# Kernel optimization log

Hardware: AMD Instinct MI355X
Metric: run time of the kernel (lower is better)

Reference implementation:

```python
import jax, jax.numpy as jnp
import numpy as np

N_ITER = 25
TOP_G = 0.07
BOT_G = 0.07
N_MIX = 1.0  # n=1 -> top target is exactly global_target


def _conv(x, W, b, stride):
    # NCHW valid conv, matching torch Conv2d
    y = jax.lax.conv_general_dilated(
        x, W, (stride, stride), 'VALID',
        dimension_numbers=('NCHW', 'OIHW', 'NCHW'))
    return y + b[None, :, None, None]


def setup_inputs() -> dict:
    key = jax.random.key(0)
    ks = jax.random.split(key, 8)
    B = 2048
    x = jax.random.normal(ks[0], (B, 3, 32, 32), jnp.float32)
    global_target = jax.random.uniform(ks[1], (B, 10), jnp.float32)

    def he(k, shape, fan_in):
        return jax.random.normal(k, shape, jnp.float32) * (1.0 / np.sqrt(fan_in))

    W1 = he(ks[2], (64, 3, 5, 5), 3 * 25);    b1 = jnp.zeros((64,), jnp.float32)
    W2 = he(ks[3], (128, 64, 5, 5), 64 * 25); b2 = jnp.zeros((128,), jnp.float32)
    W3 = he(ks[4], (256, 128, 3, 3), 128 * 9); b3 = jnp.zeros((256,), jnp.float32)
    W4 = he(ks[5], (10, 1024), 1024);          b4 = jnp.zeros((10,), jnp.float32)
    return {"x": x, "global_target": global_target,
            "W1": W1, "b1": b1, "W2": W2, "b2": b2,
            "W3": W3, "b3": b3, "W4": W4, "b4": b4}


def reference(x, global_target, W1, b1, W2, b2, W3, b3, W4, b4):
    B = x.shape[0]
    # layer functions (wts[0..3] in the torch module)
    f1 = lambda z: jax.nn.relu(_conv(z, W1, b1, 2))                      # [B,64,14,14]
    f2 = lambda z: jax.nn.relu(_conv(z, W2, b2, 2))                      # [B,128,5,5]
    f3 = lambda z: jax.nn.relu(_conv(z, W3, b3, 2)).reshape(z.shape[0], -1)  # [B,1024]
    f4 = lambda z: z @ W4.T + b4                                         # [B,10]

    # compute_values: feedforward pass
    h1 = f1(x); h2 = f2(h1); h3 = f3(h2); h4 = f4(h3)
    # top target: n*global_target + (1-n)*h4  (n=1)
    t4 = N_MIX * global_target + (1.0 - N_MIX) * h4

    # compute_PC_targets: iterative inference.
    # p[1] = wts[0](targ[0]) = f1(x) is constant == h1, so eps1 = t1 - h1.
    def step(carry, _):
        t1, t2, t3, p2, p3, p4 = carry
        e1 = t1 - h1
        e2 = t2 - p2
        e3 = t3 - p3
        e4 = (t4 - jax.nn.softmax(p4, axis=1)) * 0.5
        # epsdfdt = vjp of next layer at current target, cotangent = next eps
        _, v2 = jax.vjp(f2, t1); (g1,) = v2(e2)
        _, v3 = jax.vjp(f3, t2); (g2,) = v3(e3)
        _, v4 = jax.vjp(f4, t3); (g3,) = v4(e4)
        t1 = t1 + TOP_G * (-e1) + BOT_G * g1
        t2 = t2 + TOP_G * (-e2) + BOT_G * g2
        t3 = t3 + TOP_G * (-e3) + BOT_G * g3
        # recompute predictions from updated targets
        p2 = f2(t1); p3 = f3(t2); p4 = f4(t3)
        return (t1, t2, t3, p2, p3, p4), None

    carry0 = (h1, h2, h3, h2, h3, h4)
    (t1, t2, t3, _, _, _), _ = jax.lax.scan(step, carry0, None, length=N_ITER)

    # return refined PC targets (targ[1..3]; targ[0]=x and targ[4]=global_target are fixed)
    return jnp.concatenate(
        [t1.reshape(B, -1), t2.reshape(B, -1), t3.reshape(B, -1)], axis=1)
```

## Files before the change

kernel.cpp:

```cpp
#include <hip/hip_runtime.h>
#include <hip/hip_bf16.h>

typedef __hip_bfloat16 bf16;
typedef __attribute__((ext_vector_type(8))) short short8v;
typedef __attribute__((ext_vector_type(4))) float float4v;


__device__ __forceinline__ float b2f(bf16 v) { return __bfloat162float(v); }
__device__ __forceinline__ bf16  f2b(float v) { return __float2bfloat16(v); }
__device__ __forceinline__ float blo(unsigned u) { return __uint_as_float(u << 16); }
__device__ __forceinline__ float bhi(unsigned u) { return __uint_as_float(u & 0xffff0000u); }
__device__ __forceinline__ unsigned short fbits(float v) {
  union { bf16 b; unsigned short u; } c; c.b = f2b(v); return c.u;
}
__device__ __forceinline__ float ubf(unsigned short u) {
  return __uint_as_float(((unsigned)u) << 16);
}
__device__ __forceinline__ void gld16(const void* g, void* l) {
  __builtin_amdgcn_global_load_lds((const unsigned int*)g, (unsigned int*)l, 16, 0, 0);
}

__global__ __launch_bounds__(256) void k_prep(
    const float* __restrict__ W1, const float* __restrict__ W2,
    const float* __restrict__ W3, float* __restrict__ W1t,
    short* __restrict__ W2f, short* __restrict__ W2u,
    short* __restrict__ W3m, short* __restrict__ W3u) {
  int i = blockIdx.x * 256 + threadIdx.x;
  if (i < 4800) {
    int oc = i / 75, k = i % 75;
    W1t[k * 64 + oc] = W1[i];
  }
  if (i < 204800) {
    int oc = i / 1600, k = i % 1600, ic = k / 25, tap = k % 25;
    float w = W2[i];
    unsigned short hi = fbits(w);
    unsigned short lo = fbits(w - ubf(hi));
    W2f[(tap * 128 + oc) * 64 + (ic ^ ((oc & 7) << 3))] = (short)hi;
    W2f[204800 + (tap * 128 + oc) * 64 + (ic ^ ((oc & 7) << 3))] = (short)lo;
    W2u[(tap * 64 + ic) * 128 + (oc ^ ((ic & 7) << 3))] = (short)hi;
  }
  if (i < 294912) {
    int oc = i / 1152, k = i % 1152, ic = k / 9, tap = k % 9;
    float w = W3[i];
    unsigned short hi = fbits(w);
    unsigned short lo = fbits(w - ubf(hi));
    W3m[(tap * 256 + oc) * 128 + (ic ^ ((oc & 7) << 3))] = (short)hi;
    W3m[294912 + (tap * 256 + oc) * 128 + (ic ^ ((oc & 7) << 3))] = (short)lo;
    W3u[(tap * 128 + ic) * 256 + (oc ^ ((ic & 7) << 3))] = (short)hi;
  }
}

__global__ __launch_bounds__(512, 1) void k_conv1s(
    const float* __restrict__ x, const float* __restrict__ W1t,
    const float* __restrict__ b1, bf16* __restrict__ h1T) {
  __shared__ float xs[480 * 66];
  __shared__ float ws[4800];
  int bt = blockIdx.x, oy = blockIdx.y;
  int tid = threadIdx.x, lane = tid & 63, w8 = tid >> 6;
  int wv = w8 & 3, h = w8 >> 2;
  for (int i = tid; i < 4800; i += 512) ws[i] = W1t[i];
#pragma unroll
  for (int r = 0; r < 15; ++r) {
    int idx = r * 512 + tid;
    int col = idx / 120, q = idx % 120;
    int ic = q / 40, rem = q % 40;
    float4 v = *(const float4*)(x + (size_t)(bt * 64 + col) * 3072 +
                                ic * 1024 + oy * 64 + rem * 4);
    float* d = xs + (ic * 160 + rem * 4) * 66 + col;
    d[0] = v.x;
    d[66] = v.y;
    d[132] = v.z;
    d[198] = v.w;
  }
  __syncthreads();
  int oc0 = wv * 16;
  float acc[7][16];
#pragma unroll
  for (int o = 0; o < 7; ++o)
#pragma unroll
    for (int j = 0; j < 16; ++j) acc[o][j] = b1[oc0 + j];
  for (int ic = 0; ic < 3; ++ic)
    for (int ky = 0; ky < 5; ++ky) {
#pragma unroll
      for (int kx = 0; kx < 5; ++kx) {
        const float* wp = ws + ((ic * 25 + ky * 5 + kx) << 6) + oc0;
        float4 w0 = *(const float4*)(wp);
        float4 w1 = *(const float4*)(wp + 4);
        float4 w2 = *(const float4*)(wp + 8);
        float4 w3 = *(const float4*)(wp + 12);
        const float* xr = xs + (ic * 160 + ky * 32 + kx) * 66 + lane;
        float xv[7];
#pragma unroll
        for (int o = 0; o < 7; ++o) xv[o] = xr[(2 * (h * 7 + o)) * 66];
#pragma unroll
        for (int o = 0; o < 7; ++o) {
          float e = xv[o];
          acc[o][0] += e * w0.x;  acc[o][1] += e * w0.y;
          acc[o][2] += e * w0.z;  acc[o][3] += e * w0.w;
          acc[o][4] += e * w1.x;  acc[o][5] += e * w1.y;
          acc[o][6] += e * w1.z;  acc[o][7] += e * w1.w;
          acc[o][8] += e * w2.x;  acc[o][9] += e * w2.y;
          acc[o][10] += e * w2.z; acc[o][11] += e * w2.w;
          acc[o][12] += e * w3.x; acc[o][13] += e * w3.y;
          acc[o][14] += e * w3.z; acc[o][15] += e * w3.w;
        }
      }
    }
#pragma unroll
  for (int o = 0; o < 7; ++o) {
    int pix = oy * 14 + h * 7 + o;
    size_t tbase = ((size_t)(pix * 32 + bt)) << 12;
#pragma unroll
    for (int q = 0; q < 4; ++q) {
      ushort4 pk;
      pk.x = fbits(fmaxf(acc[o][q * 4 + 0], 0.f));
      pk.y = fbits(fmaxf(acc[o][q * 4 + 1], 0.f));
      pk.z = fbits(fmaxf(acc[o][q * 4 + 2], 0.f));
      pk.w = fbits(fmaxf(acc[o][q * 4 + 3], 0.f));
      int ocr = oc0 + q * 4;
      size_t off = tbase + lane * 64 + (ocr ^ ((lane & 7) << 3));
      *(ushort4*)(h1T + off) = pk;
    }
  }
}

__global__ __launch_bounds__(256) void k_fwd2m(
    const bf16* __restrict__ in1, const short* __restrict__ W2f,
    const float* __restrict__ b2, bf16* __restrict__ p2T,
    const bf16* __restrict__ t2e, bf16* __restrict__ e2T, int einit) {
  __shared__ __align__(16) short As0[8192];
  __shared__ __align__(16) short As1[8192];
  __shared__ __align__(16) short Bs[2][4096];
  int bid = blockIdx.x;
  int j = bid >> 3;
  int cbp = (bid & 7) * 2 + (j & 1), pos = j >> 1;
  int cb0 = cbp * 2;
  int tid = threadIdx.x, lane = tid & 63, wv = tid >> 6;
  int oy = pos / 5, ox = pos % 5;
  float4v acc[2][2][4];
#pragma unroll
  for (int c = 0; c < 2; ++c)
#pragma unroll
    for (int m = 0; m < 2; ++m)
#pragma unroll
      for (int n = 0; n < 4; ++n) acc[c][m][n] = (float4v){0.f, 0.f, 0.f, 0.f};

  for (int tap = 0; tap < 25; ++tap) {
    int ky = tap / 5, kx = tap % 5;
    int ipix = (2 * oy + ky) * 14 + (2 * ox + kx);
    __syncthreads();
    {
      const uint4* bs0 = (const uint4*)(in1 + (((size_t)(ipix * 32 + cb0)) << 12));
      const uint4* bs1 = (const uint4*)(in1 + (((size_t)(ipix * 32 + cb0 + 1)) << 12));
      uint4* bd = (uint4*)Bs;
      gld16(&bs0[tid], &bd[tid]);
      gld16(&bs0[tid + 256], &bd[tid + 256]);
      gld16(&bs1[tid], &bd[tid + 512]);
      gld16(&bs1[tid + 256], &bd[tid + 768]);
      const uint4* ah = (const uint4*)(W2f + tap * 8192);
      const uint4* al = (const uint4*)(W2f + 204800 + tap * 8192);
      uint4* dh = (uint4*)As0;
      uint4* dl = (uint4*)As1;
#pragma unroll
      for (int p = 0; p < 4; ++p) {
        gld16(&ah[tid + p * 256], &dh[tid + p * 256]);
        gld16(&al[tid + p * 256], &dl[tid + p * 256]);
      }
    }
    __syncthreads();
#pragma unroll
    for (int ks = 0; ks < 2; ++ks) {
      int ic0 = ks * 32 + ((lane >> 4) << 3);
      short8v bfr[2][4];
#pragma unroll
      for (int c = 0; c < 2; ++c)
#pragma unroll
        for (int n = 0; n < 4; ++n) {
          int colv = n * 16 + (lane & 15);
          bfr[c][n] = *(const short8v*)(&Bs[c][0] + colv * 64 + (ic0 ^ ((colv & 7) << 3)));
        }
#pragma unroll
      for (int m = 0; m < 2; ++m) {
        int row = wv * 32 + m * 16 + (lane & 15);
        int aoff = row * 64 + (ic0 ^ ((row & 7) << 3));
        short8v ah = *(const short8v*)(As0 + aoff);
        short8v al = *(const short8v*)(As1 + aoff);
#pragma unroll
        for (int c = 0; c < 2; ++c)
#pragma unroll
          for (int n = 0; n < 4; ++n) {
            acc[c][m][n] = __builtin_amdgcn_mfma_f32_16x16x32_bf16(ah, bfr[c][n], acc[c][m][n], 0, 0, 0);
            acc[c][m][n] = __builtin_amdgcn_mfma_f32_16x16x32_bf16(al, bfr[c][n], acc[c][m][n], 0, 0, 0);
          }
      }
    }
  }
#pragma unroll
  for (int c = 0; c < 2; ++c) {
    size_t tb2 = ((size_t)(pos * 32 + cb0 + c)) << 13;
#pragma unroll
    for (int m = 0; m < 2; ++m) {
      int ocb = wv * 32 + m * 16 + ((lane >> 4) << 2);
      float4 bv = *(const float4*)(b2 + ocb);
#pragma unroll
      for (int n = 0; n < 4; ++n) {
        int colv = n * 16 + (lane & 15);
        ushort4 pk;
        pk.x = fbits(fmaxf(acc[c][m][n][0] + bv.x, 0.f));
        pk.y = fbits(fmaxf(acc[c][m][n][1] + bv.y, 0.f));
        pk.z = fbits(fmaxf(acc[c][m][n][2] + bv.z, 0.f));
        pk.w = fbits(fmaxf(acc[c][m][n][3] + bv.w, 0.f));
        size_t off = tb2 + colv * 128 + (ocb ^ ((colv & 7) << 3));
        *(ushort4*)(p2T + off) = pk;
        if (einit) {
          ushort4 z = {0, 0, 0, 0};
          *(ushort4*)(e2T + off) = z;
        } else {
          ushort4 tv = *(const ushort4*)(t2e + off);
          ushort4 ev;
          float p0, t0;
          p0 = ubf(pk.x); t0 = ubf(tv.x); ev.x = fbits(p0 > 0.f ? t0 - p0 : 0.f);
          p0 = ubf(pk.y); t0 = ubf(tv.y); ev.y = fbits(p0 > 0.f ? t0 - p0 : 0.f);
          p0 = ubf(pk.z); t0 = ubf(tv.z); ev.z = fbits(p0 > 0.f ? t0 - p0 : 0.f);
          p0 = ubf(pk.w); t0 = ubf(tv.w); ev.w = fbits(p0 > 0.f ? t0 - p0 : 0.f);
          *(ushort4*)(e2T + off) = ev;
        }
      }
    }
  }
}

__global__ __launch_bounds__(256) void k_upd1m(
    const bf16* __restrict__ e2T, const short* __restrict__ W2u,
    const bf16* __restrict__ h1T, const bf16* __restrict__ t1r,
    bf16* __restrict__ t1w) {
  __shared__ __align__(16) short As0[8192];
  __shared__ __align__(16) short Es[2][8192];
  int bid = blockIdx.x;
  int j = bid >> 3;
  int cbp = (bid & 7) * 2 + (j & 1), pix = j >> 1;
  int cb0 = cbp * 2;
  int tid = threadIdx.x, lane = tid & 63, wv = tid >> 6;
  int iy = pix / 14, ix = pix % 14;
  float4v acc[2][4];
#pragma unroll
  for (int c = 0; c < 2; ++c)
#pragma unroll
    for (int n = 0; n < 4; ++n) acc[c][n] = (float4v){0.f, 0.f, 0.f, 0.f};

  for (int ky = iy & 1; ky <= 4; ky += 2) {
    int oy = (iy - ky) >> 1;
    if (oy < 0 || oy > 4) continue;
    for (int kx = ix & 1; kx <= 4; kx += 2) {
      int ox = (ix - kx) >> 1;
      if (ox < 0 || ox > 4) continue;
      int erow = oy * 5 + ox, tap = ky * 5 + kx;
      __syncthreads();
      {
        const uint4* es0 = (const uint4*)(e2T + (((size_t)(erow * 32 + cb0)) << 13));
        const uint4* es1 = (const uint4*)(e2T + (((size_t)(erow * 32 + cb0 + 1)) << 13));
        uint4* ed = (uint4*)Es;
        const uint4* ah = (const uint4*)(W2u + tap * 8192);
        uint4* dh = (uint4*)As0;
#pragma unroll
        for (int p = 0; p < 4; ++p) {
          gld16(&es0[tid + p * 256], &ed[tid + p * 256]);
          gld16(&es1[tid + p * 256], &ed[tid + p * 256 + 1024]);
          gld16(&ah[tid + p * 256], &dh[tid + p * 256]);
        }
      }
      __syncthreads();
#pragma unroll
      for (int ks = 0; ks < 4; ++ks) {
        int oc0 = ks * 32 + ((lane >> 4) << 3);
        int row = wv * 16 + (lane & 15);
        int aoff = row * 128 + (oc0 ^ ((row & 7) << 3));
        short8v ah = *(const short8v*)(As0 + aoff);
#pragma unroll
        for (int c = 0; c < 2; ++c)
#pragma unroll
          for (int n = 0; n < 4; ++n) {
            int colv = n * 16 + (lane & 15);
            short8v ef = *(const short8v*)(&Es[c][0] + colv * 128 + (oc0 ^ ((colv & 7) << 3)));
            acc[c][n] = __builtin_amdgcn_mfma_f32_16x16x32_bf16(ah, ef, acc[c][n], 0, 0, 0);
          }
      }
    }
  }
  int icb = wv * 16 + ((lane >> 4) << 2);
#pragma unroll
  for (int c = 0; c < 2; ++c) {
    size_t tb1 = ((size_t)(pix * 32 + cb0 + c)) << 12;
#pragma unroll
    for (int n = 0; n < 4; ++n) {
      int colv = n * 16 + (lane & 15);
      size_t off = tb1 + colv * 64 + (icb ^ ((colv & 7) << 3));
      ushort4 tv = *(const ushort4*)(t1r + off);
      ushort4 hv = *(const ushort4*)(h1T + off);
      ushort4 rp;
      float t0, h0;
      t0 = ubf(tv.x); h0 = ubf(hv.x);
      rp.x = fbits(t0 - 0.07f * (t0 - h0) + 0.07f * acc[c][n][0]);
      t0 = ubf(tv.y); h0 = ubf(hv.y);
      rp.y = fbits(t0 - 0.07f * (t0 - h0) + 0.07f * acc[c][n][1]);
      t0 = ubf(tv.z); h0 = ubf(hv.z);
      rp.z = fbits(t0 - 0.07f * (t0 - h0) + 0.07f * acc[c][n][2]);
      t0 = ubf(tv.w); h0 = ubf(hv.w);
      rp.w = fbits(t0 - 0.07f * (t0 - h0) + 0.07f * acc[c][n][3]);
      *(ushort4*)(t1w + off) = rp;
    }
  }
}

__global__ __launch_bounds__(256) void k_fwd3m(
    const bf16* __restrict__ in2, const short* __restrict__ W3m,
    const float* __restrict__ b3, bf16* __restrict__ p3T,
    const bf16* __restrict__ t3e, bf16* __restrict__ e3T, int einit) {
  __shared__ __align__(16) short As0[8192];
  __shared__ __align__(16) short As1[8192];
  __shared__ __align__(16) short Bs[8192];
  int bid = blockIdx.x;
  int j = bid >> 3;
  int cb = (bid & 7) * 4 + (j & 3);
  int r = j >> 2;
  int pos = r & 3, och = r >> 2;
  int tid = threadIdx.x, lane = tid & 63, wv = tid >> 6;
  int oy = pos >> 1, ox = pos & 1;
  float4v acc[4];
#pragma unroll
  for (int n = 0; n < 4; ++n) acc[n] = (float4v){0.f, 0.f, 0.f, 0.f};

  for (int tap = 0; tap < 9; ++tap) {
    int ky = tap / 3, kx = tap % 3;
    int irow = (2 * oy + ky) * 5 + (2 * ox + kx);
    __syncthreads();
    {
      const uint4* bs = (const uint4*)(in2 + (((size_t)(irow * 32 + cb)) << 13));
      uint4* bd = (uint4*)Bs;
#pragma unroll
      for (int p = 0; p < 4; ++p) gld16(&bs[tid + p * 256], &bd[tid + p * 256]);
      const uint4* ah = (const uint4*)(W3m + ((size_t)tap * 256 + och * 64) * 128);
      const uint4* al = (const uint4*)(W3m + 294912 + ((size_t)tap * 256 + och * 64) * 128);
      uint4* dh = (uint4*)As0;
      uint4* dl = (uint4*)As1;
#pragma unroll
      for (int p = 0; p < 4; ++p) {
        gld16(&ah[tid + p * 256], &dh[tid + p * 256]);
        gld16(&al[tid + p * 256], &dl[tid + p * 256]);
      }
    }
    __syncthreads();
#pragma unroll
    for (int ks = 0; ks < 4; ++ks) {
      int ic0 = ks * 32 + ((lane >> 4) << 3);
      short8v bfr[4];
#pragma unroll
      for (int n = 0; n < 4; ++n) {
        int colv = n * 16 + (lane & 15);
        bfr[n] = *(const short8v*)(Bs + colv * 128 + (ic0 ^ ((colv & 7) << 3)));
      }
      int row = wv * 16 + (lane & 15);
      int aoff = row * 128 + (ic0 ^ ((row & 7) << 3));
      short8v ah = *(const short8v*)(As0 + aoff);
      short8v al = *(const short8v*)(As1 + aoff);
#pragma unroll
      for (int n = 0; n < 4; ++n) {
        acc[n] = __builtin_amdgcn_mfma_f32_16x16x32_bf16(ah, bfr[n], acc[n], 0, 0, 0);
        acc[n] = __builtin_amdgcn_mfma_f32_16x16x32_bf16(al, bfr[n], acc[n], 0, 0, 0);
      }
    }
  }
  size_t tb3 = ((size_t)(pos * 32 + cb)) << 14;
  int ocg = och * 64 + wv * 16 + ((lane >> 4) << 2);
  float4 bv = *(const float4*)(b3 + ocg);
#pragma unroll
  for (int n = 0; n < 4; ++n) {
    int colv = n * 16 + (lane & 15);
    ushort4 pk;
    pk.x = fbits(fmaxf(acc[n][0] + bv.x, 0.f));
    pk.y = fbits(fmaxf(acc[n][1] + bv.y, 0.f));
    pk.z = fbits(fmaxf(acc[n][2] + bv.z, 0.f));
    pk.w = fbits(fmaxf(acc[n][3] + bv.w, 0.f));
    size_t off = tb3 + colv * 256 + (ocg ^ ((colv & 7) << 3));
    *(ushort4*)(p3T + off) = pk;
    if (einit) {
      ushort4 z = {0, 0, 0, 0};
      *(ushort4*)(e3T + off) = z;
    } else {
      ushort4 tv = *(const ushort4*)(t3e + off);
      ushort4 ev;
      float p0, t0;
      p0 = ubf(pk.x); t0 = ubf(tv.x); ev.x = fbits(p0 > 0.f ? t0 - p0 : 0.f);
      p0 = ubf(pk.y); t0 = ubf(tv.y); ev.y = fbits(p0 > 0.f ? t0 - p0 : 0.f);
      p0 = ubf(pk.z); t0 = ubf(tv.z); ev.z = fbits(p0 > 0.f ? t0 - p0 : 0.f);
      p0 = ubf(pk.w); t0 = ubf(tv.w); ev.w = fbits(p0 > 0.f ? t0 - p0 : 0.f);
      *(ushort4*)(e3T + off) = ev;
    }
  }
}

__global__ __launch_bounds__(256) void k_upd2m(
    const bf16* __restrict__ e3T, const bf16* __restrict__ p2T,
    const short* __restrict__ W3u, const bf16* __restrict__ t2r,
    bf16* __restrict__ t2w) {
  __shared__ __align__(16) short Es[8192];
  __shared__ __align__(16) short As0[16384];
  int bid = blockIdx.x;
  int j = bid >> 3;
  int cb = (bid & 7) * 4 + (j & 3), pix = j >> 2;
  int tid = threadIdx.x, lane = tid & 63, wv = tid >> 6;
  int iy = pix / 5, ix = pix % 5;
  float4v acc[2][4];
#pragma unroll
  for (int m = 0; m < 2; ++m)
#pragma unroll
    for (int n = 0; n < 4; ++n) acc[m][n] = (float4v){0.f, 0.f, 0.f, 0.f};

  for (int ky = iy & 1; ky <= 2; ky += 2) {
    int oy = (iy - ky) >> 1;
    if (oy < 0 || oy > 1) continue;
    for (int kx = ix & 1; kx <= 2; kx += 2) {
      int ox = (ix - kx) >> 1;
      if (ox < 0 || ox > 1) continue;
      int erow = oy * 2 + ox, tap = ky * 3 + kx;
      for (int occ = 0; occ < 2; ++occ) {
        __syncthreads();
        {
          size_t tb = ((size_t)(erow * 32 + cb)) << 14;
          uint4* ed = (uint4*)Es;
#pragma unroll
          for (int p = 0; p < 4; ++p) {
            int fi = tid + p * 256;
            int colr = fi >> 4, q = fi & 15;
            size_t g = tb + colr * 256 + occ * 128 + q * 8;
            gld16(e3T + g, &ed[fi]);
          }
          uint4* dh = (uint4*)As0;
#pragma unroll
          for (int p = 0; p < 8; ++p) {
            int fi = tid + p * 256;
            int icr = fi >> 4, q = fi & 15;
            size_t srcoff = ((size_t)(tap * 128 + icr)) * 256 + occ * 128 + q * 8;
            gld16(W3u + srcoff, &dh[fi]);
          }
        }
        __syncthreads();
#pragma unroll
        for (int ks = 0; ks < 4; ++ks) {
          int oc0 = ks * 32 + ((lane >> 4) << 3);
          short8v efr[4];
#pragma unroll
          for (int n = 0; n < 4; ++n) {
            int colv = n * 16 + (lane & 15);
            efr[n] = *(const short8v*)(Es + colv * 128 + (oc0 ^ ((colv & 7) << 3)));
          }
#pragma unroll
          for (int m = 0; m < 2; ++m) {
            int icr = wv * 32 + m * 16 + (lane & 15);
            int aoff = icr * 128 + (oc0 ^ ((icr & 7) << 3));
            short8v ah = *(const short8v*)(As0 + aoff);
#pragma unroll
            for (int n = 0; n < 4; ++n) {
              acc[m][n] = __builtin_amdgcn_mfma_f32_16x16x32_bf16(ah, efr[n], acc[m][n], 0, 0, 0);
            }
          }
        }
      }
    }
  }
  size_t tb2 = ((size_t)(pix * 32 + cb)) << 13;
#pragma unroll
  for (int m = 0; m < 2; ++m) {
    int icr = wv * 32 + m * 16 + ((lane >> 4) << 2);
#pragma unroll
    for (int n = 0; n < 4; ++n) {
      int colv = n * 16 + (lane & 15);
      size_t off = tb2 + colv * 128 + (icr ^ ((colv & 7) << 3));
      ushort4 tv = *(const ushort4*)(t2r + off);
      ushort4 pv = *(const ushort4*)(p2T + off);
      ushort4 rp;
      float t0, p0;
      t0 = ubf(tv.x); p0 = ubf(pv.x);
      rp.x = fbits(t0 - 0.07f * (t0 - p0) + 0.07f * acc[m][n][0]);
      t0 = ubf(tv.y); p0 = ubf(pv.y);
      rp.y = fbits(t0 - 0.07f * (t0 - p0) + 0.07f * acc[m][n][1]);
      t0 = ubf(tv.z); p0 = ubf(pv.z);
      rp.z = fbits(t0 - 0.07f * (t0 - p0) + 0.07f * acc[m][n][2]);
      t0 = ubf(tv.w); p0 = ubf(pv.w);
      rp.w = fbits(t0 - 0.07f * (t0 - p0) + 0.07f * acc[m][n][3]);
      *(ushort4*)(t2w + off) = rp;
    }
  }
}

__global__ __launch_bounds__(256) void k_fu3(
    const float* __restrict__ gt, const float* __restrict__ W4,
    const float* __restrict__ b4, const bf16* __restrict__ p3T,
    const bf16* __restrict__ t3r, bf16* __restrict__ t3w) {
  __shared__ __align__(16) float w4s[10560];
  int tid = threadIdx.x;
  for (int i = tid; i < 10240; i += 256) {
    int o = i >> 10, k = i & 1023;
    w4s[o * 1056 + k + ((k >> 7) << 2)] = W4[i];
  }
  __syncthreads();
  int c = blockIdx.x * 8 + (tid >> 5);
  int cb = c >> 6, colL = c & 63, subk = tid & 31;
  int pos = subk & 3, ch0 = (subk >> 2) * 32;
  int xc = (colL & 7) << 3;
  size_t boff = (((size_t)(pos * 32 + cb)) << 14) + colL * 256 + ch0;
  const bf16* trd = t3r + boff;
  const bf16* pb = p3T + boff;
  uint4 tq[4];
#pragma unroll
  for (int q = 0; q < 4; ++q) tq[q] = *(const uint4*)(trd + q * 8);
  float acc[10] = {};
#pragma unroll
  for (int q = 0; q < 4; ++q) {
    unsigned wds[4] = {tq[q].x, tq[q].y, tq[q].z, tq[q].w};
    int chb = (ch0 + q * 8) ^ xc;
#pragma unroll
    for (int h = 0; h < 4; ++h) {
      float v0 = blo(wds[h]), v1 = bhi(wds[h]);
      int k0 = (chb + 2 * h) * 4 + pos;
      int ks = k0 + ((k0 >> 7) << 2);
#pragma unroll
      for (int o = 0; o < 10; ++o)
        acc[o] += v0 * w4s[o * 1056 + ks] + v1 * w4s[o * 1056 + ks + 4];
    }
  }
#pragma unroll
  for (int off = 16; off > 0; off >>= 1)
#pragma unroll
    for (int o = 0; o < 10; ++o) acc[o] += __shfl_xor(acc[o], off, 32);
  float pv[10], m = -1e30f;
#pragma unroll
  for (int o = 0; o < 10; ++o) {
    pv[o] = acc[o] + b4[o];
    m = fmaxf(m, pv[o]);
  }
  float s = 0.f;
#pragma unroll
  for (int o = 0; o < 10; ++o) {
    pv[o] = __expf(pv[o] - m);
    s += pv[o];
  }
  float inv = 1.f / s;
  float e4[10];
#pragma unroll
  for (int o = 0; o < 10; ++o)
    e4[o] = (gt[(size_t)c * 10 + o] - pv[o] * inv) * 0.5f;
  bf16* tb = t3w + boff;
#pragma unroll
  for (int q = 0; q < 4; ++q) {
    uint4 pq = *(const uint4*)(pb + q * 8);
    unsigned tw[4] = {tq[q].x, tq[q].y, tq[q].z, tq[q].w};
    unsigned pw[4] = {pq.x, pq.y, pq.z, pq.w};
    int chb = (ch0 + q * 8) ^ xc;
    unsigned ro[4];
#pragma unroll
    for (int h = 0; h < 4; ++h) {
      int k0 = (chb + 2 * h) * 4 + pos;
      int ks = k0 + ((k0 >> 7) << 2);
      float g0 = 0.f, g1 = 0.f;
#pragma unroll
      for (int o = 0; o < 10; ++o) {
        g0 += e4[o] * w4s[o * 1056 + ks];
        g1 += e4[o] * w4s[o * 1056 + ks + 4];
      }
      float t0 = blo(tw[h]), p0 = blo(pw[h]);
      float t1 = bhi(tw[h]), p1 = bhi(pw[h]);
      float r0 = t0 - 0.07f * (t0 - p0) + 0.07f * g0;
      float r1 = t1 - 0.07f * (t1 - p1) + 0.07f * g1;
      ro[h] = (unsigned)fbits(r0) | ((unsigned)fbits(r1) << 16);
    }
    uint4 rv = {ro[0], ro[1], ro[2], ro[3]};
    *(uint4*)(tb + q * 8) = rv;
  }
}

__global__ __launch_bounds__(256) void k_tr1(
    const bf16* __restrict__ t1T, float* __restrict__ out) {
  __shared__ short lds[2 * 64 * 224];
  int cb = blockIdx.x, c0 = blockIdx.y * 2;
  int tid = threadIdx.x;
  for (int i = tid; i < 3136; i += 256) {
    int pix = i >> 4, q = i & 15;
    int colL = q >> 3, chb = (q & 7) << 3;
    int col = c0 + colL;
    uint4 v = *(const uint4*)(t1T + (((size_t)(pix * 32 + cb)) << 12) + col * 64 + chb);
    int icb = chb ^ ((col & 7) << 3);
    int posX = pix ^ (((icb >> 3) & 7) << 2);
    short* d = lds + (colL * 64 + icb) * 224 + posX;
    const short* vs = (const short*)&v;
#pragma unroll
    for (int j = 0; j < 8; ++j) d[j * 224] = vs[j];
  }
  __syncthreads();
  for (int i = tid; i < 6272; i += 256) {
    int colL = i / 3136, m = i % 3136;
    int ic = m / 49, pp = m % 49;
    int posX = (pp * 4) ^ (((ic >> 3) & 7) << 2);
    const short* s = lds + (colL * 64 + ic) * 224 + posX;
    float4 o;
    o.x = ubf((unsigned short)s[0]);
    o.y = ubf((unsigned short)s[1]);
    o.z = ubf((unsigned short)s[2]);
    o.w = ubf((unsigned short)s[3]);
    *(float4*)(out + ((size_t)(cb * 64 + c0 + colL)) * 16768 + m * 4) = o;
  }
}

__global__ __launch_bounds__(256) void k_tr2(
    const bf16* __restrict__ t2T, float* __restrict__ out) {
  __shared__ short lds[4 * 128 * 32];
  int cb = blockIdx.x, c0 = blockIdx.y * 4;
  int tid = threadIdx.x;
  for (int i = tid; i < 1600; i += 256) {
    int pos = i >> 6, q = i & 63;
    int colL = q >> 4, chb = (q & 15) << 3;
    int col = c0 + colL;
    uint4 v = *(const uint4*)(t2T + (((size_t)(pos * 32 + cb)) << 13) + col * 128 + chb);
    int ocb = chb ^ ((col & 7) << 3);
    int posX = pos ^ (((ocb >> 3) & 7) << 2);
    short* d = lds + (colL * 128 + ocb) * 32 + posX;
    const short* vs = (const short*)&v;
#pragma unroll
    for (int j = 0; j < 8; ++j) d[j * 32] = vs[j];
  }
  __syncthreads();
  for (int i = tid; i < 3200; i += 256) {
    int colL = i / 800, m = i % 800;
    int f0 = m * 4;
    float4 o;
    float* po = &o.x;
#pragma unroll
    for (int t = 0; t < 4; ++t) {
      int f = f0 + t;
      int oc = f / 25, pos = f % 25;
      int posX = pos ^ (((oc >> 3) & 7) << 2);
      po[t] = ubf((unsigned short)lds[(colL * 128 + oc) * 32 + posX]);
    }
    *(float4*)(out + ((size_t)(cb * 64 + c0 + colL)) * 16768 + 12544 + f0) = o;
  }
}

__global__ __launch_bounds__(256) void k_tr3(
    const bf16* __restrict__ t3T, float* __restrict__ out) {
  int tid = threadIdx.x;
  int sample = blockIdx.x * 8 + (tid >> 5);
  int cb = sample >> 6, col = sample & 63;
  int chb = (tid & 31) << 3;
  int icb = chb ^ ((col & 7) << 3);
  uint4 v[4];
#pragma unroll
  for (int pos = 0; pos < 4; ++pos)
    v[pos] = *(const uint4*)(t3T + (((size_t)(pos * 32 + cb)) << 14) + col * 256 + chb);
  const unsigned short* s0 = (const unsigned short*)&v[0];
  const unsigned short* s1 = (const unsigned short*)&v[1];
  const unsigned short* s2 = (const unsigned short*)&v[2];
  const unsigned short* s3 = (const unsigned short*)&v[3];
  float* ob = out + (size_t)sample * 16768 + 15744 + icb * 4;
#pragma unroll
  for (int j = 0; j < 8; ++j) {
    float4 o;
    o.x = ubf(s0[j]);
    o.y = ubf(s1[j]);
    o.z = ubf(s2[j]);
    o.w = ubf(s3[j]);
    *(float4*)(ob + j * 4) = o;
  }
}

extern "C" void kernel_launch(void* const* d_in, const int* in_sizes, int n_in,
                              void* d_out, int out_size, void* d_ws,
                              size_t ws_size, hipStream_t stream) {
  const float* x  = (const float*)d_in[0];
  const float* gt = (const float*)d_in[1];
  const float* W1 = (const float*)d_in[2];
  const float* b1 = (const float*)d_in[3];
  const float* W2 = (const float*)d_in[4];
  const float* b2 = (const float*)d_in[5];
  const float* W3 = (const float*)d_in[6];
  const float* b3 = (const float*)d_in[7];
  const float* W4 = (const float*)d_in[8];
  const float* b4 = (const float*)d_in[9];
  float* out = (float*)d_out;

  bf16* h1T = (bf16*)d_ws;
  bf16* t1T = h1T + 25690112ull;
  bf16* t2T = t1T + 25690112ull;
  bf16* p2T = t2T + 6553600ull;
  bf16* t3T = p2T + 6553600ull;
  bf16* p3T = t3T + 2097152ull;
  float* p4f = (float*)(p3T + 2097152ull);
  float* W1t = p4f + 20480;
  short* W3m = (short*)(W1t + 4800);
  short* W3u = W3m + 589824;
  short* W2f = W3u + 589824;
  short* W2u = W2f + 409600;
  bf16* e2T = (bf16*)out;
  bf16* e3T = e2T + 6553600ull;

  dim3 blk(256);

  k_prep<<<1152, blk, 0, stream>>>(W1, W2, W3, W1t, W2f, W2u, W3m, W3u);
  k_conv1s<<<dim3(32, 14), dim3(512), 0, stream>>>(x, W1t, b1, h1T);
  k_fwd2m<<<400, blk, 0, stream>>>(h1T, W2f, b2, p2T, p2T, e2T, 1);
  k_fwd3m<<<512, blk, 0, stream>>>(p2T, W3m, b3, p3T, p3T, e3T, 1);

  for (int it = 0; it < 25; ++it) {
    const bf16* t1r = (it == 0) ? h1T : t1T;
    const bf16* t2r = (it == 0) ? p2T : t2T;
    const bf16* t3r = (it == 0) ? p3T : t3T;
    k_upd1m<<<3136, blk, 0, stream>>>(e2T, W2u, h1T, t1r, t1T);
    k_upd2m<<<800, blk, 0, stream>>>(e3T, p2T, W3u, t2r, t2T);
    k_fu3<<<256, blk, 0, stream>>>(gt, W4, b4, p3T, t3r, t3T);
    if (it < 24) {
      k_fwd2m<<<400, blk, 0, stream>>>(t1T, W2f, b2, p2T, t2T, e2T, 0);
      k_fwd3m<<<512, blk, 0, stream>>>(t2T, W3m, b3, p3T, t3T, e3T, 0);
    }
  }
  k_tr1<<<dim3(32, 32), blk, 0, stream>>>(t1T, out);
  k_tr2<<<dim3(32, 16), blk, 0, stream>>>(t2T, out);
  k_tr3<<<256, blk, 0, stream>>>(t3T, out);
}
```

Measured before the change: 3.378 ms.

## Process two column blocks per block in upd2m to reuse W3 tiles

Each k_upd2m block now handles two batch column blocks instead of one, loading both error tiles into LDS while sharing a single W3 tile load and A-fragment reads across both. The grid is halved from 800 to 400 blocks. This cuts redundant W3 global loads and LDS reads per MFMA. In exchange the block doubles its accumulator registers and LDS footprint, which can lower occupancy, and 400 blocks may underfill the GPU's compute units.

```diff
diff --git a/kernel.cpp b/kernel.cpp
--- a/kernel.cpp
+++ b/kernel.cpp
@@ -403,18 +403,21 @@
     const bf16* __restrict__ e3T, const bf16* __restrict__ p2T,
     const short* __restrict__ W3u, const bf16* __restrict__ t2r,
     bf16* __restrict__ t2w) {
-  __shared__ __align__(16) short Es[8192];
+  __shared__ __align__(16) short Es[2][8192];
   __shared__ __align__(16) short As0[16384];
   int bid = blockIdx.x;
   int j = bid >> 3;
-  int cb = (bid & 7) * 4 + (j & 3), pix = j >> 2;
+  int cbp = (bid & 7) * 2 + (j & 1), pix = j >> 1;
+  int cb0 = cbp * 2;
   int tid = threadIdx.x, lane = tid & 63, wv = tid >> 6;
   int iy = pix / 5, ix = pix % 5;
-  float4v acc[2][4];
-#pragma unroll
-  for (int m = 0; m < 2; ++m)
-#pragma unroll
-    for (int n = 0; n < 4; ++n) acc[m][n] = (float4v){0.f, 0.f, 0.f, 0.f};
+  float4v acc[2][2][4];
+#pragma unroll
+  for (int c = 0; c < 2; ++c)
+#pragma unroll
+    for (int m = 0; m < 2; ++m)
+#pragma unroll
+      for (int n = 0; n < 4; ++n) acc[c][m][n] = (float4v){0.f, 0.f, 0.f, 0.f};
 
   for (int ky = iy & 1; ky <= 2; ky += 2) {
     int oy = (iy - ky) >> 1;
@@ -426,14 +429,16 @@
       for (int occ = 0; occ < 2; ++occ) {
         __syncthreads();
         {
-          size_t tb = ((size_t)(erow * 32 + cb)) << 14;
+          size_t tb0 = ((size_t)(erow * 32 + cb0)) << 14;
+          size_t tb1 = ((size_t)(erow * 32 + cb0 + 1)) << 14;
           uint4* ed = (uint4*)Es;
 #pragma unroll
           for (int p = 0; p < 4; ++p) {
             int fi = tid + p * 256;
             int colr = fi >> 4, q = fi & 15;
-            size_t g = tb + colr * 256 + occ * 128 + q * 8;
-            gld16(e3T + g, &ed[fi]);
+            size_t goff = colr * 256 + occ * 128 + q * 8;
+            gld16(e3T + tb0 + goff, &ed[fi]);
+            gld16(e3T + tb1 + goff, &ed[fi + 1024]);
           }
           uint4* dh = (uint4*)As0;
 #pragma unroll
@@ -448,47 +453,54 @@
 #pragma unroll
         for (int ks = 0; ks < 4; ++ks) {
           int oc0 = ks * 32 + ((lane >> 4) << 3);
-          short8v efr[4];
-#pragma unroll
-          for (int n = 0; n < 4; ++n) {
-            int colv = n * 16 + (lane & 15);
-            efr[n] = *(const short8v*)(Es + colv * 128 + (oc0 ^ ((colv & 7) << 3)));
-          }
+          short8v efr[2][4];
+#pragma unroll
+          for (int c = 0; c < 2; ++c)
+#pragma unroll
+            for (int n = 0; n < 4; ++n) {
+              int colv = n * 16 + (lane & 15);
+              efr[c][n] = *(const short8v*)(&Es[c][0] + colv * 128 + (oc0 ^ ((colv & 7) << 3)));
+            }
 #pragma unroll
           for (int m = 0; m < 2; ++m) {
             int icr = wv * 32 + m * 16 + (lane & 15);
             int aoff = icr * 128 + (oc0 ^ ((icr & 7) << 3));
             short8v ah = *(const short8v*)(As0 + aoff);
 #pragma unroll
-            for (int n = 0; n < 4; ++n) {
-              acc[m][n] = __builtin_amdgcn_mfma_f32_16x16x32_bf16(ah, efr[n], acc[m][n], 0, 0, 0);
-            }
+            for (int c = 0; c < 2; ++c)
+#pragma unroll
+              for (int n = 0; n < 4; ++n) {
+                acc[c][m][n] = __builtin_amdgcn_mfma_f32_16x16x32_bf16(ah, efr[c][n], acc[c][m][n], 0, 0, 0);
+              }
           }
         }
       }
     }
   }
-  size_t tb2 = ((size_t)(pix * 32 + cb)) << 13;
-#pragma unroll
-  for (int m = 0; m < 2; ++m) {
-    int icr = wv * 32 + m * 16 + ((lane >> 4) << 2);
-#pragma unroll
-    for (int n = 0; n < 4; ++n) {
-      int colv = n * 16 + (lane & 15);
-      size_t off = tb2 + colv * 128 + (icr ^ ((colv & 7) << 3));
-      ushort4 tv = *(const ushort4*)(t2r + off);
-      ushort4 pv = *(const ushort4*)(p2T + off);
-      ushort4 rp;
-      float t0, p0;
-      t0 = ubf(tv.x); p0 = ubf(pv.x);
-      rp.x = fbits(t0 - 0.07f * (t0 - p0) + 0.07f * acc[m][n][0]);
-      t0 = ubf(tv.y); p0 = ubf(pv.y);
-      rp.y = fbits(t0 - 0.07f * (t0 - p0) + 0.07f * acc[m][n][1]);
-      t0 = ubf(tv.z); p0 = ubf(pv.z);
-      rp.z = fbits(t0 - 0.07f * (t0 - p0) + 0.07f * acc[m][n][2]);
-      t0 = ubf(tv.w); p0 = ubf(pv.w);
-      rp.w = fbits(t0 - 0.07f * (t0 - p0) + 0.07f * acc[m][n][3]);
-      *(ushort4*)(t2w + off) = rp;
+#pragma unroll
+  for (int c = 0; c < 2; ++c) {
+    size_t tb2 = ((size_t)(pix * 32 + cb0 + c)) << 13;
+#pragma unroll
+    for (int m = 0; m < 2; ++m) {
+      int icr = wv * 32 + m * 16 + ((lane >> 4) << 2);
+#pragma unroll
+      for (int n = 0; n < 4; ++n) {
+        int colv = n * 16 + (lane & 15);
+        size_t off = tb2 + colv * 128 + (icr ^ ((colv & 7) << 3));
+        ushort4 tv = *(const ushort4*)(t2r + off);
+        ushort4 pv = *(const ushort4*)(p2T + off);
+        ushort4 rp;
+        float t0, p0;
+        t0 = ubf(tv.x); p0 = ubf(pv.x);
+        rp.x = fbits(t0 - 0.07f * (t0 - p0) + 0.07f * acc[c][m][n][0]);
+        t0 = ubf(tv.y); p0 = ubf(pv.y);
+        rp.y = fbits(t0 - 0.07f * (t0 - p0) + 0.07f * acc[c][m][n][1]);
+        t0 = ubf(tv.z); p0 = ubf(pv.z);
+        rp.z = fbits(t0 - 0.07f * (t0 - p0) + 0.07f * acc[c][m][n][2]);
+        t0 = ubf(tv.w); p0 = ubf(pv.w);
+        rp.w = fbits(t0 - 0.07f * (t0 - p0) + 0.07f * acc[c][m][n][3]);
+        *(ushort4*)(t2w + off) = rp;
+      }
     }
   }
 }
@@ -714,7 +726,7 @@
     const bf16* t2r = (it == 0) ? p2T : t2T;
     const bf16* t3r = (it == 0) ? p3T : t3T;
     k_upd1m<<<3136, blk, 0, stream>>>(e2T, W2u, h1T, t1r, t1T);
-    k_upd2m<<<800, blk, 0, stream>>>(e3T, p2T, W3u, t2r, t2T);
+    k_upd2m<<<400, blk, 0, stream>>>(e3T, p2T, W3u, t2r, t2T);
     k_fu3<<<256, blk, 0, stream>>>(gt, W4, b4, p3T, t3r, t3T);
     if (it < 24) {
       k_fwd2m<<<400, blk, 0, stream>>>(t1T, W2f, b2, p2T, t2T, e2T, 0);
```

After: 3.425 ms. No clear change (+1.4%).
